# Kernel tuning notes

Hardware: AMD Instinct MI355X
Metric: run time of the kernel (lower is better)

The kernel has to match this reference:

```python
import jax, jax.numpy as jnp
import numpy as np

N = 100000   # nodes
E = 600000   # edges per relation
D = 128      # input_dim == output_dim, num_heads = 1
NEG_SLOPE = 0.2  # DGL GATConv default leaky_relu slope


def setup_inputs() -> dict:
    key = jax.random.key(0)
    ks = jax.random.split(key, 10)
    scale = 1.0 / np.sqrt(D)
    return {
        "feat_src": jax.random.normal(ks[0], (N, D), jnp.float32) * 0.1,
        "feat_dst": jax.random.normal(ks[1], (N, D), jnp.float32) * 0.1,
        "intra_src": jax.random.randint(ks[2], (E,), 0, N, jnp.int32),
        "intra_dst": jax.random.randint(ks[3], (E,), 0, N, jnp.int32),
        "inter_src": jax.random.randint(ks[4], (E,), 0, N, jnp.int32),
        "inter_dst": jax.random.randint(ks[5], (E,), 0, N, jnp.int32),
        # 8 GATConvs: conv{1..4} x {intra1, inter}
        "W": jax.random.normal(ks[6], (8, D, D), jnp.float32) * scale,
        "attn_l": jax.random.normal(ks[7], (8, D), jnp.float32) * scale,
        "attn_r": jax.random.normal(ks[8], (8, D), jnp.float32) * scale,
        "bias": jnp.zeros((8, D), jnp.float32),
        "lam": jnp.full((4,), 0.5, jnp.float32),  # lamda1..lamda4
        "n_nodes": N,
    }


def _gat(x_src, x_dst, src, dst, W, al, ar, b, n):
    # DGL GATConv, 1 head, residual=Identity (in==out), no dropout, no activation
    hs = x_src @ W                      # [N, D]
    hd = x_dst @ W                      # [N, D]
    el = hs @ al                        # [N]
    er = hd @ ar                        # [N]
    e = jax.nn.leaky_relu(el[src] + er[dst], NEG_SLOPE)   # [E]
    m = jax.ops.segment_max(e, dst, num_segments=n)
    m = jnp.where(jnp.isfinite(m), m, 0.0)                # empty segments -> 0
    ex = jnp.exp(e - m[dst])
    den = jax.ops.segment_sum(ex, dst, num_segments=n)
    alpha = ex / jnp.maximum(den[dst], 1e-9)              # edge softmax over dst
    agg = jax.ops.segment_sum(alpha[:, None] * hs[src], dst, num_segments=n)
    return agg + x_dst + b              # attention aggregate + residual + bias


def reference(feat_src, feat_dst, intra_src, intra_dst, inter_src, inter_dst,
              W, attn_l, attn_r, bias, lam, n_nodes):
    fwd = ((intra_src, intra_dst), (inter_src, inter_dst))
    rev = ((intra_dst, intra_src), (inter_dst, inter_src))  # g.reverse()

    def conv(xs, xd, edges, i0, i1):
        (s0, d0), (s1, d1) = edges
        # HeteroGraphConv aggregate='sum' over the two relations
        return (_gat(xs, xd, s0, d0, W[i0], attn_l[i0], attn_r[i0], bias[i0], n_nodes)
                + _gat(xs, xd, s1, d1, W[i1], attn_l[i1], attn_r[i1], bias[i1], n_nodes))

    h10 = conv(feat_src, feat_dst, fwd, 0, 1)   # conv1(g, (src, dst))
    h11 = conv(feat_dst, feat_dst, fwd, 2, 3)   # conv2(g, (dst, dst))
    h20 = conv(feat_src, feat_dst, rev, 4, 5)   # conv3(g.rev, (src, dst))
    h21 = conv(feat_dst, feat_dst, rev, 6, 7)   # conv4(g.rev, (dst, dst))

    # hybrid: hl = l1*h10 + l2*h11 ; hr = l3*h20 + l4*h21 ; h = hl + hr
    # head dim is 1 so the max over heads is the identity -> [N, D]
    return lam[0] * h10 + lam[1] * h11 + lam[2] * h20 + lam[3] * h21
```

## Files before the change

### kernel.cpp

```cpp
#include <hip/hip_runtime.h>
#include <hip/hip_bf16.h>

typedef unsigned short ushort_t;
typedef __bf16 bf16x8 __attribute__((ext_vector_type(8)));
typedef ushort_t u16x8 __attribute__((ext_vector_type(8)));
typedef unsigned int u32x4 __attribute__((ext_vector_type(4)));
typedef float f32x4 __attribute__((ext_vector_type(4)));
typedef float f32x2 __attribute__((ext_vector_type(2)));

__device__ __forceinline__ float bf2f(ushort_t u){ return __uint_as_float(((unsigned)u)<<16); }
__device__ __forceinline__ ushort_t f2bf(float f){
  unsigned x = __float_as_uint(f);
  unsigned r = (x + 0x7fffu + ((x>>16)&1u)) >> 16;
  return (ushort_t)r;
}

__global__ __launch_bounds__(256) void init_kernel(const float* __restrict__ W,
    const float* __restrict__ al, const float* __restrict__ ar,
    const float* __restrict__ bias, const float* __restrict__ lam,
    float* __restrict__ wl, float* __restrict__ wr, float* __restrict__ bsum,
    ushort_t* __restrict__ Wf, int* __restrict__ counts, int n) {
  int b = blockIdx.x;
  if (b < 8) {
    int i = b, j = threadIdx.x;
    if (j < 128) {
      const float* Wi  = W + ((size_t)i*128 + j)*128;
      const float* ali = al + i*128;
      const float* ari = ar + i*128;
      float sl = 0.f, sr = 0.f;
      for (int k = 0; k < 128; ++k) { float w = Wi[k]; sl += w*ali[k]; sr += w*ari[k]; }
      wl[i*128+j] = sl; wr[i*128+j] = sr;
      if (i == 0) {
        float bb = 0.f;
        for (int t = 0; t < 8; ++t) bb += lam[t>>1]*bias[t*128+j];
        bsum[j] = bb;
      }
    }
  } else if (b < 72) {
    int tid = (b-8)*256 + threadIdx.x;
    int gat  = tid >> 11;
    int kk   = (tid >> 9) & 3;
    int f    = (tid >> 6) & 7;
    int lane = tid & 63;
    float c = lam[gat >> 1];
    int krow = kk*32 + (lane >> 4)*8;
    int col  = f*16 + (lane & 15);
    ushort_t v[8];
#pragma unroll
    for (int i = 0; i < 8; ++i)
      v[i] = f2bf(c * W[((size_t)gat*128 + krow + i)*128 + col]);
    ushort_t* o = Wf + (size_t)tid*8;
#pragma unroll
    for (int i = 0; i < 8; ++i) o[i] = v[i];
  } else {
    int idx = ((b-72)*256 + threadIdx.x)*4;
    int total = 4*n;
    if (idx + 4 <= total) {
      int4 z = {0,0,0,0};
      *(int4*)(counts + idx) = z;
    } else {
      for (int q = idx; q < total; ++q) counts[q] = 0;
    }
  }
}

__global__ __launch_bounds__(256) void prep_hist_kernel(const float* __restrict__ fs,
    const float* __restrict__ fd, const float* __restrict__ wl, const float* __restrict__ wr,
    float* __restrict__ att, ushort_t* __restrict__ fb,
    const int* __restrict__ ia_s, const int* __restrict__ ia_d,
    const int* __restrict__ ie_s, const int* __restrict__ ie_d,
    int* __restrict__ counts, int n, int e, int n8, int npb, int G) {
  int b = blockIdx.x;
  if (b < npb) {
    int wid  = (b*256 + threadIdx.x) >> 6;
    int lane = threadIdx.x & 63;
    if (wid >= n) return;
    float2 s = *(const float2*)(fs + (size_t)wid*128 + lane*2);
    float2 d = *(const float2*)(fd + (size_t)wid*128 + lane*2);
    ushort2 us; us.x = f2bf(s.x); us.y = f2bf(s.y);
    ushort2 ud; ud.x = f2bf(d.x); ud.y = f2bf(d.y);
    *(ushort2*)(fb + (size_t)wid*256 + lane*2) = us;
    *(ushort2*)(fb + (size_t)wid*256 + 128 + lane*2) = ud;
#pragma unroll
    for (int i = 0; i < 8; ++i) {
      float2 wlv = *(const float2*)(wl + i*128 + lane*2);
      float2 wrv = *(const float2*)(wr + i*128 + lane*2);
      bool use_s = (i==0)||(i==1)||(i==4)||(i==5);
      float xx = use_s ? s.x : d.x;
      float xy = use_s ? s.y : d.y;
      float vl = xx*wlv.x + xy*wlv.y;
      float vr = d.x*wrv.x + d.y*wrv.y;
#pragma unroll
      for (int off = 32; off; off >>= 1) { vl += __shfl_xor(vl, off); vr += __shfl_xor(vr, off); }
      if (lane == 0) { att[(size_t)wid*16 + i] = vl; att[(size_t)wid*16 + 8 + i] = vr; }
    }
  } else {
    int bid = b - npb;
    int x = bid & 7;
    int lo = x*n8, hi = lo + n8; if (hi > n) hi = n;
    int tid = (bid >> 3)*256 + threadIdx.x;
    int nthr = G << 8;
#pragma unroll
    for (int g = 0; g < 4; ++g) {
      const int* dp = (g==0) ? ia_d : (g==1) ? ie_d : (g==2) ? ia_s : ie_s;
      int bo = g*n;
      for (int i = tid*4; i < e; i += nthr*4) {
        if (i + 4 <= e) {
          int4 d4 = *(const int4*)(dp + i);
          if (d4.x >= lo && d4.x < hi) atomicAdd(&counts[bo + d4.x], 1);
          if (d4.y >= lo && d4.y < hi) atomicAdd(&counts[bo + d4.y], 1);
          if (d4.z >= lo && d4.z < hi) atomicAdd(&counts[bo + d4.z], 1);
          if (d4.w >= lo && d4.w < hi) atomicAdd(&counts[bo + d4.w], 1);
        } else {
          for (int q = i; q < e; ++q) {
            int dv = dp[q];
            if (dv >= lo && dv < hi) atomicAdd(&counts[bo + dv], 1);
          }
        }
      }
    }
  }
}

__global__ __launch_bounds__(256) void scan_local_kernel(const int* __restrict__ counts,
    int* __restrict__ rowptr, int* __restrict__ bsums, int total) {
  __shared__ int sh[256];
  int base = blockIdx.x*1024;
  int tid = threadIdx.x;
  int v[4]; int s = 0;
#pragma unroll
  for (int q = 0; q < 4; ++q) { int idx = base + tid*4 + q; int x = (idx < total) ? counts[idx] : 0; v[q] = x; s += x; }
  sh[tid] = s; __syncthreads();
  for (int off = 1; off < 256; off <<= 1) {
    int t2 = (tid >= off) ? sh[tid-off] : 0;
    __syncthreads();
    sh[tid] += t2;
    __syncthreads();
  }
  if (tid == 255) bsums[blockIdx.x] = sh[255];
  int run = sh[tid] - s;
#pragma unroll
  for (int q = 0; q < 4; ++q) { int idx = base + tid*4 + q; if (idx < total) rowptr[idx] = run; run += v[q]; }
}

__global__ __launch_bounds__(512) void scan_finish_kernel(int* __restrict__ rowptr,
    int* __restrict__ cursor, const int* __restrict__ bsums, int total, int nb, int grand) {
  __shared__ int sb[1024];
  __shared__ int ps[512];
  int tid = threadIdx.x;
  int v0 = (2*tid   < nb) ? bsums[2*tid]   : 0;
  int v1 = (2*tid+1 < nb) ? bsums[2*tid+1] : 0;
  int s = v0 + v1;
  ps[tid] = s; __syncthreads();
  for (int off = 1; off < 512; off <<= 1) {
    int t2 = (tid >= off) ? ps[tid-off] : 0;
    __syncthreads();
    ps[tid] += t2;
    __syncthreads();
  }
  int excl = ps[tid] - s;
  sb[2*tid] = excl; sb[2*tid+1] = excl + v0;
  __syncthreads();
  int idx = blockIdx.x*512 + tid;
  if (idx < total) {
    int v = rowptr[idx] + sb[idx >> 10];
    rowptr[idx] = v;
    cursor[idx] = v;
  }
  if (idx == total) rowptr[total] = grand;
}

__global__ __launch_bounds__(256) void fill_kernel(const int* __restrict__ ia_s,
    const int* __restrict__ ia_d, const int* __restrict__ ie_s, const int* __restrict__ ie_d,
    const float* __restrict__ att, int* __restrict__ cursor, int2* __restrict__ epk,
    int n, int e, int n8, int G) {
  int bid = blockIdx.x;
  int x = bid & 7;
  int lo = x*n8, hi = lo + n8; if (hi > n) hi = n;
  int tid = (bid >> 3)*256 + threadIdx.x;
  int nthr = G << 8;
#pragma unroll
  for (int g = 0; g < 4; ++g) {
    const int* dp = (g==0) ? ia_d : (g==1) ? ie_d : (g==2) ? ia_s : ie_s;
    const int* sp = (g==0) ? ia_s : (g==1) ? ie_s : (g==2) ? ia_d : ie_d;
    int gatA = (g < 2) ? g : g + 2;
    int gatB = gatA + 2;
    int bo = g*n;
    for (int i = tid*4; i < e; i += nthr*4) {
      int lim = (i + 4 <= e) ? 4 : (e - i);
      if (lim == 4) {
        int4 d4 = *(const int4*)(dp + i);
        bool m0 = d4.x >= lo && d4.x < hi;
        bool m1 = d4.y >= lo && d4.y < hi;
        bool m2 = d4.z >= lo && d4.z < hi;
        bool m3 = d4.w >= lo && d4.w < hi;
        if (m0 | m1 | m2 | m3) {
          int4 s4 = *(const int4*)(sp + i);
          int dv[4] = {d4.x, d4.y, d4.z, d4.w};
          int sv[4] = {s4.x, s4.y, s4.z, s4.w};
          bool mv[4] = {m0, m1, m2, m3};
#pragma unroll
          for (int q = 0; q < 4; ++q) {
            if (mv[q]) {
              int dd = dv[q], ss = sv[q];
              float ea = att[(size_t)ss*16 + gatA] + att[(size_t)dd*16 + 8 + gatA];
              float eb = att[(size_t)ss*16 + gatB] + att[(size_t)dd*16 + 8 + gatB];
              ea = (ea > 0.f) ? ea : 0.2f*ea;
              eb = (eb > 0.f) ? eb : 0.2f*eb;
              unsigned p2 = (unsigned)f2bf(__expf(ea)) | ((unsigned)f2bf(__expf(eb)) << 16);
              int pos = atomicAdd(&cursor[bo + dd], 1);
              epk[pos] = make_int2(ss, (int)p2);
            }
          }
        }
      } else {
        for (int q = i; q < e; ++q) {
          int dd = dp[q];
          if (dd >= lo && dd < hi) {
            int ss = sp[q];
            float ea = att[(size_t)ss*16 + gatA] + att[(size_t)dd*16 + 8 + gatA];
            float eb = att[(size_t)ss*16 + gatB] + att[(size_t)dd*16 + 8 + gatB];
            ea = (ea > 0.f) ? ea : 0.2f*ea;
            eb = (eb > 0.f) ? eb : 0.2f*eb;
            unsigned p2 = (unsigned)f2bf(__expf(ea)) | ((unsigned)f2bf(__expf(eb)) << 16);
            int pos = atomicAdd(&cursor[bo + dd], 1);
            epk[pos] = make_int2(ss, (int)p2);
          }
        }
      }
    }
  }
}

__global__ __launch_bounds__(512) void fused_kernel(const ushort_t* __restrict__ fb,
    const int* __restrict__ rowptr, const int2* __restrict__ epk,
    const ushort_t* __restrict__ Wf, const float* __restrict__ lam,
    const float* __restrict__ bsum, float* __restrict__ out, int n) {
  __shared__ ushort_t As[16*1024];
  int t = threadIdx.x, w = t >> 6, lane = t & 63;
  int base = blockIdx.x*16;
  int g = w >> 1;
  int half = lane >> 5;
  int l    = lane & 31;
  int typ  = (l >> 4) & 1;

  for (int i = 0; i < 8; ++i) {
    int di = (w & 1)*8 + i;
    int d = base + di; if (d >= n) d = n - 1;
    int row = rowptr[(size_t)g*n + d], end = rowptr[(size_t)g*n + d + 1];
    f32x2 acc0 = {0.f,0.f}, acc1 = {0.f,0.f}, acc2 = {0.f,0.f}, acc3 = {0.f,0.f};
    float den = 0.f;
    int e2 = row + half;
    int2 eC = {0, 0}; u32x4 uC = {0,0,0,0};
    if (e2 < end) {
      eC = epk[e2];
      uC = *reinterpret_cast<const u32x4*>(fb + (size_t)eC.x*256 + l*8);
    }
    while (e2 < end) {
      int eN = e2 + 2;
      int2 eT = eC; u32x4 uN = uC;
      if (eN < end) {
        eT = epk[eN];
        uN = *reinterpret_cast<const u32x4*>(fb + (size_t)eT.x*256 + l*8);
      }
      unsigned p2 = (unsigned)eC.y;
      float p = typ ? __uint_as_float(p2 & 0xffff0000u)
                    : __uint_as_float(p2 << 16);
      den += p;
      f32x2 pv = {p, p};
      f32x2 x0, x1, x2, x3;
      x0[0] = __uint_as_float(uC[0] << 16); x0[1] = __uint_as_float(uC[0] & 0xffff0000u);
      x1[0] = __uint_as_float(uC[1] << 16); x1[1] = __uint_as_float(uC[1] & 0xffff0000u);
      x2[0] = __uint_as_float(uC[2] << 16); x2[1] = __uint_as_float(uC[2] & 0xffff0000u);
      x3[0] = __uint_as_float(uC[3] << 16); x3[1] = __uint_as_float(uC[3] & 0xffff0000u);
      acc0 += pv*x0; acc1 += pv*x1; acc2 += pv*x2; acc3 += pv*x3;
      e2 = eN; eC = eT; uC = uN;
    }
    den += __shfl_xor(den, 32);
    acc0[0] += __shfl_xor(acc0[0], 32); acc0[1] += __shfl_xor(acc0[1], 32);
    acc1[0] += __shfl_xor(acc1[0], 32); acc1[1] += __shfl_xor(acc1[1], 32);
    acc2[0] += __shfl_xor(acc2[0], 32); acc2[1] += __shfl_xor(acc2[1], 32);
    acc3[0] += __shfl_xor(acc3[0], 32); acc3[1] += __shfl_xor(acc3[1], 32);
    if (half == 0) {
      float r = 1.f/fmaxf(den, 1e-9f);
      u16x8 o;
      o[0]=f2bf(acc0[0]*r); o[1]=f2bf(acc0[1]*r); o[2]=f2bf(acc1[0]*r); o[3]=f2bf(acc1[1]*r);
      o[4]=f2bf(acc2[0]*r); o[5]=f2bf(acc2[1]*r); o[6]=f2bf(acc3[0]*r); o[7]=f2bf(acc3[1]*r);
      int k = g*256 + l*8;
      int idx = di*1024 + (k ^ ((di & 7) << 3));
      *reinterpret_cast<u16x8*>(As + idx) = o;
    }
  }
  __syncthreads();

  int lr = lane & 15, lg = lane >> 4;
  f32x4 c0 = {0.f,0.f,0.f,0.f};
#pragma unroll
  for (int ks = 0; ks < 32; ++ks) {
    int kc = ks*32 + lg*8;
    int idx = lr*1024 + (kc ^ ((lr & 7) << 3));
    bf16x8 a = *reinterpret_cast<const bf16x8*>(As + idx);
    int wp = ks >> 3, sub = ks & 7;
    int gg = ((sub >= 4) ? 2 : 0) + ((wp < 2) ? wp : wp + 2);
    int kk = sub & 3;
    const ushort_t* bp = Wf + (((size_t)(gg*4 + kk)*8 + w)*64 + lane)*8;
    bf16x8 b0 = *reinterpret_cast<const bf16x8*>(bp);
    c0 = __builtin_amdgcn_mfma_f32_16x16x32_bf16(a, b0, c0, 0, 0, 0);
  }
  float rc = 2.f*(lam[0] + lam[1] + lam[2] + lam[3]);
  int gc = w*16 + lr;
#pragma unroll
  for (int r2 = 0; r2 < 4; ++r2) {
    int gr = base + lg*4 + r2;
    if (gr < n) {
      size_t o = (size_t)gr*128 + gc;
      float fdv = bf2f(fb[(size_t)gr*256 + 128 + gc]);
      out[o] = c0[r2] + rc*fdv + bsum[gc];
    }
  }
}

extern "C" void kernel_launch(void* const* d_in, const int* in_sizes, int n_in,
                              void* d_out, int out_size, void* d_ws, size_t ws_size,
                              hipStream_t stream) {
  const float* fs  = (const float*)d_in[0];
  const float* fd  = (const float*)d_in[1];
  const int* ia_s  = (const int*)d_in[2];
  const int* ia_d  = (const int*)d_in[3];
  const int* ie_s  = (const int*)d_in[4];
  const int* ie_d  = (const int*)d_in[5];
  const float* W   = (const float*)d_in[6];
  const float* al  = (const float*)d_in[7];
  const float* ar  = (const float*)d_in[8];
  const float* bias= (const float*)d_in[9];
  const float* lam = (const float*)d_in[10];
  int n = in_sizes[0] / 128;
  int e = in_sizes[2];
  float* out = (float*)d_out;

  char* ws = (char*)d_ws;
  size_t off = 0;
  auto alloc = [&](size_t bytes) -> char* { char* p = ws + off; off += (bytes + 255) & ~(size_t)255; return p; };
  float* wl      = (float*)alloc((size_t)8*128*4);
  float* wr      = (float*)alloc((size_t)8*128*4);
  float* bsum    = (float*)alloc(128*4);
  float* att     = (float*)alloc((size_t)n*16*4);
  int*   counts  = (int*)alloc((size_t)4*n*4);
  int*   rowptr  = (int*)alloc(((size_t)4*n + 1)*4);
  int*   bsums   = (int*)alloc(4096);
  int2*  epk     = (int2*)alloc((size_t)4*e*8);
  ushort_t* Wf   = (ushort_t*)alloc((size_t)8*128*128*2);
  ushort_t* fb   = (ushort_t*)alloc((size_t)n*256*2);
  (void)ws_size; (void)n_in; (void)out_size;

  int n8 = (n + 7)/8;
  int total = 4*n;
  int nb = (total + 1023)/1024;
  int nZ = (total + 1023)/1024;
  int npb = (n + 3)/4;
  int G = 160;

  hipLaunchKernelGGL(init_kernel, dim3(72 + nZ), dim3(256), 0, stream,
                     W, al, ar, bias, lam, wl, wr, bsum, Wf, counts, n);
  hipLaunchKernelGGL(prep_hist_kernel, dim3(npb + 8*G), dim3(256), 0, stream,
                     fs, fd, wl, wr, att, fb, ia_s, ia_d, ie_s, ie_d,
                     counts, n, e, n8, npb, G);
  hipLaunchKernelGGL(scan_local_kernel, dim3(nb), dim3(256), 0, stream,
                     counts, rowptr, bsums, total);
  hipLaunchKernelGGL(scan_finish_kernel, dim3((total + 512)/512), dim3(512), 0, stream,
                     rowptr, counts, bsums, total, nb, 4*e);
  hipLaunchKernelGGL(fill_kernel, dim3(8*G), dim3(256), 0, stream,
                     ia_s, ia_d, ie_s, ie_d, att, counts, epk, n, e, n8, G);
  hipLaunchKernelGGL(fused_kernel, dim3((n+15)/16), dim3(512), 0, stream,
                     fb, rowptr, epk, Wf, lam, bsum, out, n);
}
```

Baseline: 706.1 us.

## Store gathered features in fp8 and regroup attention logits per edge group

Node features used in the edge gather are now stored as fp8 (e4m3) instead of bf16, which halves the bytes read per edge in the aggregation loop. The attention logits are laid out as per-group float2 arrays, so each edge in the fill kernel does one 8-byte load for the source side and one for the destination side instead of four scattered loads. The residual now reads the original fp32 feat_dst. The risk is fp8 quantisation error in the aggregated features, which may exceed the accuracy tolerance.

Result: faster. 659.1 us (-6.7%).

```diff
diff --git a/kernel.cpp b/kernel.cpp
--- a/kernel.cpp
+++ b/kernel.cpp
@@ -2,9 +2,10 @@
 #include <hip/hip_bf16.h>
 
 typedef unsigned short ushort_t;
+typedef unsigned char uchar_t;
 typedef __bf16 bf16x8 __attribute__((ext_vector_type(8)));
 typedef ushort_t u16x8 __attribute__((ext_vector_type(8)));
-typedef unsigned int u32x4 __attribute__((ext_vector_type(4)));
+typedef unsigned int u32x2 __attribute__((ext_vector_type(2)));
 typedef float f32x4 __attribute__((ext_vector_type(4)));
 typedef float f32x2 __attribute__((ext_vector_type(2)));
 
@@ -66,7 +67,7 @@
 
 __global__ __launch_bounds__(256) void prep_hist_kernel(const float* __restrict__ fs,
     const float* __restrict__ fd, const float* __restrict__ wl, const float* __restrict__ wr,
-    float* __restrict__ att, ushort_t* __restrict__ fb,
+    float2* __restrict__ attg, float2* __restrict__ erg, uchar_t* __restrict__ fb8,
     const int* __restrict__ ia_s, const int* __restrict__ ia_d,
     const int* __restrict__ ie_s, const int* __restrict__ ie_d,
     int* __restrict__ counts, int n, int e, int n8, int npb, int G) {
@@ -77,10 +78,11 @@
     if (wid >= n) return;
     float2 s = *(const float2*)(fs + (size_t)wid*128 + lane*2);
     float2 d = *(const float2*)(fd + (size_t)wid*128 + lane*2);
-    ushort2 us; us.x = f2bf(s.x); us.y = f2bf(s.y);
-    ushort2 ud; ud.x = f2bf(d.x); ud.y = f2bf(d.y);
-    *(ushort2*)(fb + (size_t)wid*256 + lane*2) = us;
-    *(ushort2*)(fb + (size_t)wid*256 + 128 + lane*2) = ud;
+    unsigned ps = (unsigned)__builtin_amdgcn_cvt_pk_fp8_f32(s.x, s.y, 0, false);
+    unsigned pd = (unsigned)__builtin_amdgcn_cvt_pk_fp8_f32(d.x, d.y, 0, false);
+    *(ushort_t*)(fb8 + (size_t)wid*256 + lane*2) = (ushort_t)(ps & 0xffffu);
+    *(ushort_t*)(fb8 + (size_t)wid*256 + 128 + lane*2) = (ushort_t)(pd & 0xffffu);
+    float elv[8], erv[8];
 #pragma unroll
     for (int i = 0; i < 8; ++i) {
       float2 wlv = *(const float2*)(wl + i*128 + lane*2);
@@ -92,7 +94,17 @@
       float vr = d.x*wrv.x + d.y*wrv.y;
 #pragma unroll
       for (int off = 32; off; off >>= 1) { vl += __shfl_xor(vl, off); vr += __shfl_xor(vr, off); }
-      if (lane == 0) { att[(size_t)wid*16 + i] = vl; att[(size_t)wid*16 + 8 + i] = vr; }
+      elv[i] = vl; erv[i] = vr;
+    }
+    if (lane == 0) {
+      attg[0*(size_t)n + wid] = make_float2(elv[0], elv[2]);
+      attg[1*(size_t)n + wid] = make_float2(elv[1], elv[3]);
+      attg[2*(size_t)n + wid] = make_float2(elv[4], elv[6]);
+      attg[3*(size_t)n + wid] = make_float2(elv[5], elv[7]);
+      erg[0*(size_t)n + wid] = make_float2(erv[0], erv[2]);
+      erg[1*(size_t)n + wid] = make_float2(erv[1], erv[3]);
+      erg[2*(size_t)n + wid] = make_float2(erv[4], erv[6]);
+      erg[3*(size_t)n + wid] = make_float2(erv[5], erv[7]);
     }
   } else {
     int bid = b - npb;
@@ -172,7 +184,8 @@
 
 __global__ __launch_bounds__(256) void fill_kernel(const int* __restrict__ ia_s,
     const int* __restrict__ ia_d, const int* __restrict__ ie_s, const int* __restrict__ ie_d,
-    const float* __restrict__ att, int* __restrict__ cursor, int2* __restrict__ epk,
+    const float2* __restrict__ attg, const float2* __restrict__ erg,
+    int* __restrict__ cursor, int2* __restrict__ epk,
     int n, int e, int n8, int G) {
   int bid = blockIdx.x;
   int x = bid & 7;
@@ -183,9 +196,9 @@
   for (int g = 0; g < 4; ++g) {
     const int* dp = (g==0) ? ia_d : (g==1) ? ie_d : (g==2) ? ia_s : ie_s;
     const int* sp = (g==0) ? ia_s : (g==1) ? ie_s : (g==2) ? ia_d : ie_d;
-    int gatA = (g < 2) ? g : g + 2;
-    int gatB = gatA + 2;
     int bo = g*n;
+    const float2* ag = attg + (size_t)g*n;
+    const float2* eg = erg + (size_t)g*n;
     for (int i = tid*4; i < e; i += nthr*4) {
       int lim = (i + 4 <= e) ? 4 : (e - i);
       if (lim == 4) {
@@ -203,8 +216,10 @@
           for (int q = 0; q < 4; ++q) {
             if (mv[q]) {
               int dd = dv[q], ss = sv[q];
-              float ea = att[(size_t)ss*16 + gatA] + att[(size_t)dd*16 + 8 + gatA];
-              float eb = att[(size_t)ss*16 + gatB] + att[(size_t)dd*16 + 8 + gatB];
+              float2 a2 = ag[ss];
+              float2 e2 = eg[dd];
+              float ea = a2.x + e2.x;
+              float eb = a2.y + e2.y;
               ea = (ea > 0.f) ? ea : 0.2f*ea;
               eb = (eb > 0.f) ? eb : 0.2f*eb;
               unsigned p2 = (unsigned)f2bf(__expf(ea)) | ((unsigned)f2bf(__expf(eb)) << 16);
@@ -218,8 +233,10 @@
           int dd = dp[q];
           if (dd >= lo && dd < hi) {
             int ss = sp[q];
-            float ea = att[(size_t)ss*16 + gatA] + att[(size_t)dd*16 + 8 + gatA];
-            float eb = att[(size_t)ss*16 + gatB] + att[(size_t)dd*16 + 8 + gatB];
+            float2 a2 = ag[ss];
+            float2 e2 = eg[dd];
+            float ea = a2.x + e2.x;
+            float eb = a2.y + e2.y;
             ea = (ea > 0.f) ? ea : 0.2f*ea;
             eb = (eb > 0.f) ? eb : 0.2f*eb;
             unsigned p2 = (unsigned)f2bf(__expf(ea)) | ((unsigned)f2bf(__expf(eb)) << 16);
@@ -232,10 +249,11 @@
   }
 }
 
-__global__ __launch_bounds__(512) void fused_kernel(const ushort_t* __restrict__ fb,
+__global__ __launch_bounds__(512) void fused_kernel(const uchar_t* __restrict__ fb8,
     const int* __restrict__ rowptr, const int2* __restrict__ epk,
     const ushort_t* __restrict__ Wf, const float* __restrict__ lam,
-    const float* __restrict__ bsum, float* __restrict__ out, int n) {
+    const float* __restrict__ fd, const float* __restrict__ bsum,
+    float* __restrict__ out, int n) {
   __shared__ ushort_t As[16*1024];
   int t = threadIdx.x, w = t >> 6, lane = t & 63;
   int base = blockIdx.x*16;
@@ -243,6 +261,7 @@
   int half = lane >> 5;
   int l    = lane & 31;
   int typ  = (l >> 4) & 1;
+  int boff = typ*128 + (l & 15)*8;
 
   for (int i = 0; i < 8; ++i) {
     int di = (w & 1)*8 + i;
@@ -251,28 +270,27 @@
     f32x2 acc0 = {0.f,0.f}, acc1 = {0.f,0.f}, acc2 = {0.f,0.f}, acc3 = {0.f,0.f};
     float den = 0.f;
     int e2 = row + half;
-    int2 eC = {0, 0}; u32x4 uC = {0,0,0,0};
+    int2 eC = {0, 0}; u32x2 uC = {0,0};
     if (e2 < end) {
       eC = epk[e2];
-      uC = *reinterpret_cast<const u32x4*>(fb + (size_t)eC.x*256 + l*8);
+      uC = *reinterpret_cast<const u32x2*>(fb8 + (size_t)eC.x*256 + boff);
     }
     while (e2 < end) {
       int eN = e2 + 2;
-      int2 eT = eC; u32x4 uN = uC;
+      int2 eT = eC; u32x2 uN = uC;
       if (eN < end) {
         eT = epk[eN];
-        uN = *reinterpret_cast<const u32x4*>(fb + (size_t)eT.x*256 + l*8);
+        uN = *reinterpret_cast<const u32x2*>(fb8 + (size_t)eT.x*256 + boff);
       }
       unsigned p2 = (unsigned)eC.y;
       float p = typ ? __uint_as_float(p2 & 0xffff0000u)
                     : __uint_as_float(p2 << 16);
       den += p;
       f32x2 pv = {p, p};
-      f32x2 x0, x1, x2, x3;
-      x0[0] = __uint_as_float(uC[0] << 16); x0[1] = __uint_as_float(uC[0] & 0xffff0000u);
-      x1[0] = __uint_as_float(uC[1] << 16); x1[1] = __uint_as_float(uC[1] & 0xffff0000u);
-      x2[0] = __uint_as_float(uC[2] << 16); x2[1] = __uint_as_float(uC[2] & 0xffff0000u);
-      x3[0] = __uint_as_float(uC[3] << 16); x3[1] = __uint_as_float(uC[3] & 0xffff0000u);
+      f32x2 x0 = __builtin_amdgcn_cvt_pk_f32_fp8((int)uC[0], false);
+      f32x2 x1 = __builtin_amdgcn_cvt_pk_f32_fp8((int)uC[0], true);
+      f32x2 x2 = __builtin_amdgcn_cvt_pk_f32_fp8((int)uC[1], false);
+      f32x2 x3 = __builtin_amdgcn_cvt_pk_f32_fp8((int)uC[1], true);
       acc0 += pv*x0; acc1 += pv*x1; acc2 += pv*x2; acc3 += pv*x3;
       e2 = eN; eC = eT; uC = uN;
     }
@@ -314,8 +332,7 @@
     int gr = base + lg*4 + r2;
     if (gr < n) {
       size_t o = (size_t)gr*128 + gc;
-      float fdv = bf2f(fb[(size_t)gr*256 + 128 + gc]);
-      out[o] = c0[r2] + rc*fdv + bsum[gc];
+      out[o] = c0[r2] + rc*fd[o] + bsum[gc];
     }
   }
 }
@@ -344,13 +361,14 @@
   float* wl      = (float*)alloc((size_t)8*128*4);
   float* wr      = (float*)alloc((size_t)8*128*4);
   float* bsum    = (float*)alloc(128*4);
-  float* att     = (float*)alloc((size_t)n*16*4);
+  float2* attg   = (float2*)alloc((size_t)4*n*8);
+  float2* erg    = (float2*)alloc((size_t)4*n*8);
   int*   counts  = (int*)alloc((size_t)4*n*4);
   int*   rowptr  = (int*)alloc(((size_t)4*n + 1)*4);
   int*   bsums   = (int*)alloc(4096);
   int2*  epk     = (int2*)alloc((size_t)4*e*8);
   ushort_t* Wf   = (ushort_t*)alloc((size_t)8*128*128*2);
-  ushort_t* fb   = (ushort_t*)alloc((size_t)n*256*2);
+  uchar_t* fb8   = (uchar_t*)alloc((size_t)n*256);
   (void)ws_size; (void)n_in; (void)out_size;
 
   int n8 = (n + 7)/8;
@@ -363,14 +381,14 @@
   hipLaunchKernelGGL(init_kernel, dim3(72 + nZ), dim3(256), 0, stream,
                      W, al, ar, bias, lam, wl, wr, bsum, Wf, counts, n);
   hipLaunchKernelGGL(prep_hist_kernel, dim3(npb + 8*G), dim3(256), 0, stream,
-                     fs, fd, wl, wr, att, fb, ia_s, ia_d, ie_s, ie_d,
+                     fs, fd, wl, wr, attg, erg, fb8, ia_s, ia_d, ie_s, ie_d,
                      counts, n, e, n8, npb, G);
   hipLaunchKernelGGL(scan_local_kernel, dim3(nb), dim3(256), 0, stream,
                      counts, rowptr, bsums, total);
   hipLaunchKernelGGL(scan_finish_kernel, dim3((total + 512)/512), dim3(512), 0, stream,
                      rowptr, counts, bsums, total, nb, 4*e);
   hipLaunchKernelGGL(fill_kernel, dim3(8*G), dim3(256), 0, stream,
-                     ia_s, ia_d, ie_s, ie_d, att, counts, epk, n, e, n8, G);
+                     ia_s, ia_d, ie_s, ie_d, attg, erg, counts, epk, n, e, n8, G);
   hipLaunchKernelGGL(fused_kernel, dim3((n+15)/16), dim3(512), 0, stream,
-                     fb, rowptr, epk, Wf, lam, bsum, out, n);
-}
+                     fb8, rowptr, epk, Wf, lam, fd, bsum, out, n);
+}
```
